# Kernel optimization log

Measured on AMD Instinct MI355X. Metric: run time of the kernel, lower is better.

Reference implementation:

```python
import jax, jax.numpy as jnp
import numpy as np

LN_EPS = 1e-5


def setup_inputs() -> dict:
    key = jax.random.key(0)
    k_h, k_s, k_d, k_w = jax.random.split(key, 4)
    N, E, F_IN, F_OUT = 100000, 1600000, 128, 128
    h = jax.random.normal(k_h, (N, F_IN), dtype=jnp.float32)
    src = jax.random.randint(k_s, (E,), 0, N, dtype=jnp.int32)
    dst = jax.random.randint(k_d, (E,), 0, N, dtype=jnp.int32)
    # Linear(2*in_feats, out_feats): weight [out, 2*in], bias [out]
    W = jax.random.normal(k_w, (F_OUT, 2 * F_IN), dtype=jnp.float32) * (1.0 / np.sqrt(2 * F_IN))
    b = jnp.zeros((F_OUT,), dtype=jnp.float32)
    gamma = jnp.ones((F_OUT,), dtype=jnp.float32)
    beta = jnp.zeros((F_OUT,), dtype=jnp.float32)
    return {"h": h, "src": src, "dst": dst, "W": W, "b": b, "gamma": gamma, "beta": beta}


def reference(h, src, dst, W, b, gamma, beta):
    N = h.shape[0]
    # mean aggregation: update_all(copy_src('h','m'), mean('m','h'))
    msg_sum = jax.ops.segment_sum(h[src], dst, num_segments=N)          # [N, F]
    deg = jax.ops.segment_sum(jnp.ones_like(dst, dtype=h.dtype), dst, num_segments=N)  # [N]
    ah = msg_sum / jnp.maximum(deg, 1.0)[:, None]                        # zero-degree -> 0 (DGL mean gives 0)
    # concat + linear
    hc = jnp.concatenate([h, ah], axis=1)                                # [N, 2F]
    z = hc @ W.T + b                                                     # [N, out]
    # LayerNorm (elementwise affine)
    mu = jnp.mean(z, axis=-1, keepdims=True)
    var = jnp.mean((z - mu) ** 2, axis=-1, keepdims=True)
    z = (z - mu) * jax.lax.rsqrt(var + LN_EPS) * gamma + beta
    # activation = relu
    return jax.nn.relu(z)
```

## Files before the change

### kernel.cpp

```cpp
#include <hip/hip_runtime.h>
#include <stdint.h>

#define FDIM 128
#define NBITS 6
#define BNODES 64
#define CAP 1536
#define PBATCH 8192

typedef __attribute__((ext_vector_type(8))) short bf16x8;
typedef __attribute__((ext_vector_type(4))) float f32x4;
typedef __attribute__((ext_vector_type(8))) unsigned short u16x8;

__device__ __forceinline__ unsigned short f32_to_bf16(float f) {
  union { float f; uint32_t u; } v; v.f = f;
  uint32_t u = v.u;
  u += 0x7FFFu + ((u >> 16) & 1u);
  return (unsigned short)(u >> 16);
}
__device__ __forceinline__ float u32lo_bf16(uint32_t u) {
  union { uint32_t u; float f; } v; v.u = u << 16; return v.f;
}
__device__ __forceinline__ float u32hi_bf16(uint32_t u) {
  union { uint32_t u; float f; } v; v.u = u & 0xFFFF0000u; return v.f;
}

__device__ __forceinline__ void gload_lds16(const void* g, void* l) {
  __builtin_amdgcn_global_load_lds(
      (const __attribute__((address_space(1))) void*)g,
      (__attribute__((address_space(3))) void*)l, 16, 0, 0);
}

__global__ void cvt_bf16_8(const float* __restrict__ in, unsigned short* __restrict__ o, int n8) {
  int i = blockIdx.x * blockDim.x + threadIdx.x;
  if (i >= n8) return;
  float4 a = ((const float4*)in)[i * 2], b = ((const float4*)in)[i * 2 + 1];
  u16x8 r;
  r[0] = f32_to_bf16(a.x); r[1] = f32_to_bf16(a.y); r[2] = f32_to_bf16(a.z); r[3] = f32_to_bf16(a.w);
  r[4] = f32_to_bf16(b.x); r[5] = f32_to_bf16(b.y); r[6] = f32_to_bf16(b.z); r[7] = f32_to_bf16(b.w);
  ((u16x8*)o)[i] = r;
}

__global__ __launch_bounds__(256) void partition_edges(
    const int* __restrict__ src, const int* __restrict__ dst,
    int* __restrict__ gcur, unsigned int* __restrict__ pairs, int E, int nbk) {
  __shared__ int hist[1600];
  for (int k = threadIdx.x; k < nbk; k += 256) hist[k] = 0;
  __syncthreads();
  int base = blockIdx.x * PBATCH;
  const int4* d4p = (const int4*)(dst + base);
  const int4* s4p = (const int4*)(src + base);
#pragma unroll
  for (int j = 0; j < PBATCH / 1024; ++j) {
    int vi = j * 256 + threadIdx.x;
    int i0 = base + vi * 4;
    if (i0 < E) {
      int4 d = d4p[vi];
      atomicAdd(&hist[d.x >> NBITS], 1);
      if (i0 + 1 < E) atomicAdd(&hist[d.y >> NBITS], 1);
      if (i0 + 2 < E) atomicAdd(&hist[d.z >> NBITS], 1);
      if (i0 + 3 < E) atomicAdd(&hist[d.w >> NBITS], 1);
    }
  }
  __syncthreads();
  for (int k = threadIdx.x; k < nbk; k += 256) {
    int c = hist[k];
    hist[k] = (c > 0) ? atomicAdd(&gcur[k], c) : 0;
  }
  __syncthreads();
#pragma unroll
  for (int j = 0; j < PBATCH / 1024; ++j) {
    int vi = j * 256 + threadIdx.x;
    int i0 = base + vi * 4;
    if (i0 < E) {
      int4 d = d4p[vi];
      int4 s = s4p[vi];
#pragma unroll
      for (int q = 0; q < 4; ++q) {
        if (i0 + q >= E) break;
        int dd = (q == 0) ? d.x : (q == 1) ? d.y : (q == 2) ? d.z : d.w;
        int ss = (q == 0) ? s.x : (q == 1) ? s.y : (q == 2) ? s.z : s.w;
        int b = dd >> NBITS;
        int pos = atomicAdd(&hist[b], 1);
        if (pos < CAP)
          pairs[(size_t)b * CAP + pos] = ((unsigned)ss << NBITS) | (unsigned)(dd & (BNODES - 1));
      }
    }
  }
}

__global__ __launch_bounds__(256) void fine_sort(
    const int* __restrict__ gcur, unsigned int* __restrict__ pairs,
    int* __restrict__ noff, int* __restrict__ ndeg, int N) {
  __shared__ int larr[CAP];
  __shared__ int sorted_[CAP];
  __shared__ int cnt[BNODES];
  __shared__ int off[BNODES];
  __shared__ int cur[BNODES];
  int b = blockIdx.x;
  int n0 = b << NBITS;
  int tid = threadIdx.x;
  int ec = gcur[b]; if (ec > CAP) ec = CAP;
  if (tid < BNODES) cnt[tid] = 0;
  unsigned int* pb = pairs + (size_t)b * CAP;
  for (int e = tid; e < ec; e += 256) larr[e] = (int)pb[e];
  __syncthreads();
  for (int e = tid; e < ec; e += 256) atomicAdd(&cnt[larr[e] & (BNODES - 1)], 1);
  __syncthreads();
  if (tid < BNODES) off[tid] = cnt[tid];
  __syncthreads();
  for (int s = 1; s < BNODES; s <<= 1) {
    int v = 0;
    if (tid < BNODES && tid >= s) v = off[tid - s];
    __syncthreads();
    if (tid < BNODES) off[tid] += v;
    __syncthreads();
  }
  if (tid < BNODES) { int e0 = off[tid] - cnt[tid]; off[tid] = e0; cur[tid] = e0; }
  __syncthreads();
  for (int e = tid; e < ec; e += 256) {
    int p = larr[e];
    int pos = atomicAdd(&cur[p & (BNODES - 1)], 1);
    sorted_[pos] = p >> NBITS;
  }
  __syncthreads();
  for (int e = tid; e < ec; e += 256) pb[e] = (unsigned int)sorted_[e];
  if (tid < BNODES) {
    int node = n0 + tid;
    if (node < N) { noff[node] = b * CAP + off[tid]; ndeg[node] = cnt[tid]; }
  }
}

__global__ __launch_bounds__(256) void gather_mean(
    const unsigned short* __restrict__ h2, const int* __restrict__ noff,
    const int* __restrict__ ndeg, const unsigned int* __restrict__ ssrc,
    unsigned short* __restrict__ ah2, int N) {
  int node = blockIdx.x * 16 + (threadIdx.x >> 4);
  int lane = threadIdx.x & 15;
  if (node >= N) return;
  int o = noff[node], d = ndeg[node];
  const uint4* h4 = (const uint4*)h2;
  float l0[4] = {0,0,0,0}, h0[4] = {0,0,0,0}, l1[4] = {0,0,0,0}, h1[4] = {0,0,0,0};
  float l2[4] = {0,0,0,0}, h2a[4] = {0,0,0,0}, l3[4] = {0,0,0,0}, h3[4] = {0,0,0,0};
  int e = 0;
  for (; e + 8 <= d; e += 8) {
    int s0 = ssrc[o + e],     s1 = ssrc[o + e + 1], s2 = ssrc[o + e + 2], s3 = ssrc[o + e + 3];
    int s4 = ssrc[o + e + 4], s5 = ssrc[o + e + 5], s6 = ssrc[o + e + 6], s7 = ssrc[o + e + 7];
    uint4 v0 = h4[(size_t)s0 * 16 + lane], v1 = h4[(size_t)s1 * 16 + lane];
    uint4 v2 = h4[(size_t)s2 * 16 + lane], v3 = h4[(size_t)s3 * 16 + lane];
    uint4 v4 = h4[(size_t)s4 * 16 + lane], v5 = h4[(size_t)s5 * 16 + lane];
    uint4 v6 = h4[(size_t)s6 * 16 + lane], v7 = h4[(size_t)s7 * 16 + lane];
    uint32_t u;
#define ACC(vv, LL, HH)                                              \
    u = vv.x; LL[0] += u32lo_bf16(u); HH[0] += u32hi_bf16(u);        \
    u = vv.y; LL[1] += u32lo_bf16(u); HH[1] += u32hi_bf16(u);        \
    u = vv.z; LL[2] += u32lo_bf16(u); HH[2] += u32hi_bf16(u);        \
    u = vv.w; LL[3] += u32lo_bf16(u); HH[3] += u32hi_bf16(u);
    ACC(v0, l0, h0) ACC(v1, l1, h1) ACC(v2, l2, h2a) ACC(v3, l3, h3)
    ACC(v4, l0, h0) ACC(v5, l1, h1) ACC(v6, l2, h2a) ACC(v7, l3, h3)
  }
  for (; e + 4 <= d; e += 4) {
    int s0 = ssrc[o + e], s1 = ssrc[o + e + 1], s2 = ssrc[o + e + 2], s3 = ssrc[o + e + 3];
    uint4 v0 = h4[(size_t)s0 * 16 + lane], v1 = h4[(size_t)s1 * 16 + lane];
    uint4 v2 = h4[(size_t)s2 * 16 + lane], v3 = h4[(size_t)s3 * 16 + lane];
    uint32_t u;
    ACC(v0, l0, h0) ACC(v1, l1, h1) ACC(v2, l2, h2a) ACC(v3, l3, h3)
  }
  for (; e < d; ++e) {
    int s0 = ssrc[o + e];
    uint4 v0 = h4[(size_t)s0 * 16 + lane];
    uint32_t u;
    ACC(v0, l0, h0)
#undef ACC
  }
  float inv = 1.0f / (float)(d > 0 ? d : 1);
  u16x8 r;
#pragma unroll
  for (int q = 0; q < 4; ++q) {
    r[2 * q]     = f32_to_bf16(((l0[q] + l1[q]) + (l2[q] + l3[q])) * inv);
    r[2 * q + 1] = f32_to_bf16(((h0[q] + h1[q]) + (h2a[q] + h3[q])) * inv);
  }
  *(u16x8*)(ah2 + (size_t)node * 128 + lane * 8) = r;
}

__global__ __launch_bounds__(256) void gemm_mfma_ln_relu(
    const unsigned short* __restrict__ h2, const unsigned short* __restrict__ ah2,
    const unsigned short* __restrict__ W2, const float* __restrict__ bias,
    const float* __restrict__ gamma, const float* __restrict__ beta,
    float* __restrict__ out, int N) {
  __shared__ unsigned short As[128 * 64];
  __shared__ unsigned short Ws[128 * 64];
  int tid = threadIdx.x;
  int w = tid >> 6, l = tid & 63;
  int lr = l & 15, lg = l >> 4;
  int n0 = blockIdx.x * 128;

  f32x4 acc[2][8];
#pragma unroll
  for (int rt = 0; rt < 2; ++rt)
#pragma unroll
    for (int ct = 0; ct < 8; ++ct) acc[rt][ct] = (f32x4){0.f, 0.f, 0.f, 0.f};

  for (int kt = 0; kt < 4; ++kt) {
    const unsigned short* abase = (kt < 2) ? h2 : ah2;
#pragma unroll
    for (int rd = 0; rd < 4; ++rd) {
      int off = rd * 4096 + tid * 16;
      int r = off >> 7;
      int s = (off >> 4) & 7;
      int ls = s ^ (r & 7);
      int gn = n0 + r; if (gn > N - 1) gn = N - 1;
      gload_lds16((const char*)abase + (size_t)gn * 256 + (size_t)(kt & 1) * 128 + ls * 16,
                  (char*)As + off);
      gload_lds16((const char*)W2 + (size_t)r * 512 + (size_t)kt * 128 + ls * 16,
                  (char*)Ws + off);
    }
    __syncthreads();

    bf16x8 aF[2][2], bF[8][2];
#pragma unroll
    for (int rt = 0; rt < 2; ++rt)
#pragma unroll
      for (int kc = 0; kc < 2; ++kc) {
        int r = w * 32 + rt * 16 + lr;
        int slot = kc * 4 + lg;
        aF[rt][kc] = *(const bf16x8*)((const char*)As + r * 128 + ((slot ^ (r & 7)) * 16));
      }
#pragma unroll
    for (int ct = 0; ct < 8; ++ct)
#pragma unroll
      for (int kc = 0; kc < 2; ++kc) {
        int r = ct * 16 + lr;
        int slot = kc * 4 + lg;
        bF[ct][kc] = *(const bf16x8*)((const char*)Ws + r * 128 + ((slot ^ (r & 7)) * 16));
      }
#pragma unroll
    for (int rt = 0; rt < 2; ++rt)
#pragma unroll
      for (int ct = 0; ct < 8; ++ct)
#pragma unroll
        for (int kc = 0; kc < 2; ++kc)
          acc[rt][ct] = __builtin_amdgcn_mfma_f32_16x16x32_bf16(
              aF[rt][kc], bF[ct][kc], acc[rt][ct], 0, 0, 0);
    __syncthreads();
  }

  float bj[8], gj[8], tj[8];
#pragma unroll
  for (int ct = 0; ct < 8; ++ct) {
    int c = ct * 16 + lr;
    bj[ct] = bias[c]; gj[ct] = gamma[c]; tj[ct] = beta[c];
  }
#pragma unroll
  for (int rt = 0; rt < 2; ++rt)
#pragma unroll
    for (int q = 0; q < 4; ++q) {
      int n = n0 + w * 32 + rt * 16 + lg * 4 + q;
      float v[8], s = 0.f, s2 = 0.f;
#pragma unroll
      for (int ct = 0; ct < 8; ++ct) {
        v[ct] = acc[rt][ct][q] + bj[ct];
        s += v[ct]; s2 += v[ct] * v[ct];
      }
#pragma unroll
      for (int off = 1; off < 16; off <<= 1) {
        s  += __shfl_xor(s, off);
        s2 += __shfl_xor(s2, off);
      }
      float mean = s * (1.f / 128.f);
      float var = s2 * (1.f / 128.f) - mean * mean;
      float rstd = rsqrtf(var + 1e-5f);
      if (n < N) {
#pragma unroll
        for (int ct = 0; ct < 8; ++ct) {
          float o = (v[ct] - mean) * rstd * gj[ct] + tj[ct];
          out[(size_t)n * FDIM + ct * 16 + lr] = fmaxf(o, 0.f);
        }
      }
    }
}

extern "C" void kernel_launch(void* const* d_in, const int* in_sizes, int n_in,
                              void* d_out, int out_size, void* d_ws, size_t ws_size,
                              hipStream_t stream) {
  const float* h     = (const float*)d_in[0];
  const int*   src   = (const int*)d_in[1];
  const int*   dst   = (const int*)d_in[2];
  const float* W     = (const float*)d_in[3];
  const float* bias  = (const float*)d_in[4];
  const float* gamma = (const float*)d_in[5];
  const float* beta  = (const float*)d_in[6];
  float* out = (float*)d_out;
  int N = in_sizes[0] / FDIM;
  int E = in_sizes[1];
  int nbk = (N + BNODES - 1) >> NBITS;

  int* gcur = (int*)d_ws;
  int* noff = (int*)((char*)d_ws + 8192);
  int* ndeg = noff + ((N + 63) / 64) * 64;
  unsigned int* pairs = (unsigned int*)(ndeg + ((N + 63) / 64) * 64);
  unsigned short* h2  = (unsigned short*)((char*)pairs + (size_t)nbk * CAP * 4);
  unsigned short* ah2 = h2 + (size_t)N * 128;
  unsigned short* W2  = ah2 + (size_t)N * 128;

  hipMemsetAsync(gcur, 0, (size_t)nbk * 4, stream);
  cvt_bf16_8<<<(N * FDIM / 8 + 255) / 256, 256, 0, stream>>>(h, h2, N * FDIM / 8);
  cvt_bf16_8<<<(FDIM * 2 * FDIM / 8 + 255) / 256, 256, 0, stream>>>(W, W2, FDIM * 2 * FDIM / 8);
  partition_edges<<<(E + PBATCH - 1) / PBATCH, 256, 0, stream>>>(src, dst, gcur, pairs, E, nbk);
  fine_sort<<<nbk, 256, 0, stream>>>(gcur, pairs, noff, ndeg, N);
  gather_mean<<<(N + 15) / 16, 256, 0, stream>>>(h2, noff, ndeg, pairs, ah2, N);
  gemm_mfma_ln_relu<<<(N + 127) / 128, 256, 0, stream>>>(h2, ah2, W2, bias, gamma, beta, out, N);
}
```

Baseline: 234.4 us.

## Replace atomic bucket partition with two-level LDS radix sort and padded gather

Result: slower. 258.5 us (+10.3%).

```diff
diff --git a/kernel.cpp b/kernel.cpp
--- a/kernel.cpp
+++ b/kernel.cpp
@@ -2,10 +2,11 @@
 #include <stdint.h>
 
 #define FDIM 128
-#define NBITS 6
-#define BNODES 64
-#define CAP 1536
+#define NB1BITS 9
+#define B1NODES 512
 #define PBATCH 8192
+#define LCAP 12288
+#define PCAP 16384
 
 typedef __attribute__((ext_vector_type(8))) short bf16x8;
 typedef __attribute__((ext_vector_type(4))) float f32x4;
@@ -40,93 +41,114 @@
   ((u16x8*)o)[i] = r;
 }
 
-__global__ __launch_bounds__(256) void partition_edges(
+__global__ __launch_bounds__(256) void l1_partition(
     const int* __restrict__ src, const int* __restrict__ dst,
-    int* __restrict__ gcur, unsigned int* __restrict__ pairs, int E, int nbk) {
-  __shared__ int hist[1600];
-  for (int k = threadIdx.x; k < nbk; k += 256) hist[k] = 0;
-  __syncthreads();
-  int base = blockIdx.x * PBATCH;
-  const int4* d4p = (const int4*)(dst + base);
-  const int4* s4p = (const int4*)(src + base);
-#pragma unroll
-  for (int j = 0; j < PBATCH / 1024; ++j) {
-    int vi = j * 256 + threadIdx.x;
-    int i0 = base + vi * 4;
-    if (i0 < E) {
-      int4 d = d4p[vi];
-      atomicAdd(&hist[d.x >> NBITS], 1);
-      if (i0 + 1 < E) atomicAdd(&hist[d.y >> NBITS], 1);
-      if (i0 + 2 < E) atomicAdd(&hist[d.z >> NBITS], 1);
-      if (i0 + 3 < E) atomicAdd(&hist[d.w >> NBITS], 1);
+    unsigned int* __restrict__ l1buf, int* __restrict__ starts, int E, int nbk1) {
+  __shared__ int hist[256];
+  __shared__ int sc[256];
+  __shared__ int cur[256];
+  __shared__ unsigned int sorted[PBATCH];
+  int tid = threadIdx.x;
+  int b0 = blockIdx.x * PBATCH;
+  int n = E - b0; if (n > PBATCH) n = PBATCH;
+  hist[tid] = 0;
+  __syncthreads();
+  for (int e = tid; e < n; e += 256) atomicAdd(&hist[dst[b0 + e] >> NB1BITS], 1);
+  __syncthreads();
+  sc[tid] = hist[tid];
+  __syncthreads();
+  for (int s = 1; s < 256; s <<= 1) {
+    int x = (tid >= s) ? sc[tid - s] : 0;
+    __syncthreads();
+    sc[tid] += x;
+    __syncthreads();
+  }
+  int excl = sc[tid] - hist[tid];
+  cur[tid] = excl;
+  __syncthreads();
+  for (int e = tid; e < n; e += 256) {
+    int d = dst[b0 + e], s = src[b0 + e];
+    int b = d >> NB1BITS;
+    int pos = atomicAdd(&cur[b], 1);
+    sorted[pos] = ((unsigned)s << NB1BITS) | (unsigned)(d & (B1NODES - 1));
+  }
+  __syncthreads();
+  unsigned int* chunk = l1buf + (size_t)blockIdx.x * PBATCH;
+  for (int e = tid; e < n; e += 256) chunk[e] = sorted[e];
+  starts[blockIdx.x * 256 + tid] = excl;
+}
+
+__global__ __launch_bounds__(256) void l2_sort(
+    const unsigned int* __restrict__ l1buf, const int* __restrict__ starts,
+    unsigned int* __restrict__ ssrc, int* __restrict__ noff, int* __restrict__ ndeg,
+    int N, int nl1b) {
+  __shared__ int sbeg[256], slen[256], scl[256];
+  __shared__ unsigned int edges[LCAP];
+  __shared__ int cnt[512], ps[512], pexcl[512], cur2[512];
+  __shared__ int ecs;
+  int b = blockIdx.x;
+  int tid = threadIdx.x;
+  int s0 = 0, len = 0;
+  if (tid < nl1b) {
+    s0 = starts[tid * 256 + b];
+    len = starts[tid * 256 + b + 1] - s0;
+  }
+  sbeg[tid] = s0; slen[tid] = len; scl[tid] = len;
+  __syncthreads();
+  for (int s = 1; s < 256; s <<= 1) {
+    int x = (tid >= s) ? scl[tid - s] : 0;
+    __syncthreads();
+    scl[tid] += x;
+    __syncthreads();
+  }
+  if (tid == 255) { int t = scl[255]; ecs = (t > LCAP) ? LCAP : t; }
+  __syncthreads();
+  int ec = ecs;
+  int wv = tid >> 6, ln = tid & 63;
+  for (int i = wv; i < nl1b; i += 4) {
+    int l = slen[i];
+    int dsto = scl[i] - l;
+    const unsigned int* seg = l1buf + (size_t)i * PBATCH + sbeg[i];
+    for (int j = ln; j < l; j += 64) {
+      int p = dsto + j;
+      if (p < LCAP) edges[p] = seg[j];
     }
   }
-  __syncthreads();
-  for (int k = threadIdx.x; k < nbk; k += 256) {
-    int c = hist[k];
-    hist[k] = (c > 0) ? atomicAdd(&gcur[k], c) : 0;
-  }
-  __syncthreads();
-#pragma unroll
-  for (int j = 0; j < PBATCH / 1024; ++j) {
-    int vi = j * 256 + threadIdx.x;
-    int i0 = base + vi * 4;
-    if (i0 < E) {
-      int4 d = d4p[vi];
-      int4 s = s4p[vi];
-#pragma unroll
-      for (int q = 0; q < 4; ++q) {
-        if (i0 + q >= E) break;
-        int dd = (q == 0) ? d.x : (q == 1) ? d.y : (q == 2) ? d.z : d.w;
-        int ss = (q == 0) ? s.x : (q == 1) ? s.y : (q == 2) ? s.z : s.w;
-        int b = dd >> NBITS;
-        int pos = atomicAdd(&hist[b], 1);
-        if (pos < CAP)
-          pairs[(size_t)b * CAP + pos] = ((unsigned)ss << NBITS) | (unsigned)(dd & (BNODES - 1));
-      }
-    }
-  }
-}
-
-__global__ __launch_bounds__(256) void fine_sort(
-    const int* __restrict__ gcur, unsigned int* __restrict__ pairs,
-    int* __restrict__ noff, int* __restrict__ ndeg, int N) {
-  __shared__ int larr[CAP];
-  __shared__ int sorted_[CAP];
-  __shared__ int cnt[BNODES];
-  __shared__ int off[BNODES];
-  __shared__ int cur[BNODES];
-  int b = blockIdx.x;
-  int n0 = b << NBITS;
-  int tid = threadIdx.x;
-  int ec = gcur[b]; if (ec > CAP) ec = CAP;
-  if (tid < BNODES) cnt[tid] = 0;
-  unsigned int* pb = pairs + (size_t)b * CAP;
-  for (int e = tid; e < ec; e += 256) larr[e] = (int)pb[e];
-  __syncthreads();
-  for (int e = tid; e < ec; e += 256) atomicAdd(&cnt[larr[e] & (BNODES - 1)], 1);
-  __syncthreads();
-  if (tid < BNODES) off[tid] = cnt[tid];
-  __syncthreads();
-  for (int s = 1; s < BNODES; s <<= 1) {
-    int v = 0;
-    if (tid < BNODES && tid >= s) v = off[tid - s];
-    __syncthreads();
-    if (tid < BNODES) off[tid] += v;
-    __syncthreads();
-  }
-  if (tid < BNODES) { int e0 = off[tid] - cnt[tid]; off[tid] = e0; cur[tid] = e0; }
-  __syncthreads();
+  cnt[tid] = 0; cnt[tid + 256] = 0;
+  __syncthreads();
+  for (int e = tid; e < ec; e += 256) atomicAdd(&cnt[edges[e] & (B1NODES - 1)], 1);
+  __syncthreads();
+  ps[tid] = (cnt[tid] + 7) & ~7;
+  ps[tid + 256] = (cnt[tid + 256] + 7) & ~7;
+  __syncthreads();
+  for (int s = 1; s < 512; s <<= 1) {
+    int i0 = tid, i1 = tid + 256;
+    int v0 = (i0 >= s) ? ps[i0 - s] : 0;
+    int v1 = (i1 >= s) ? ps[i1 - s] : 0;
+    __syncthreads();
+    ps[i0] += v0; ps[i1] += v1;
+    __syncthreads();
+  }
+  pexcl[tid] = ps[tid] - ((cnt[tid] + 7) & ~7);
+  pexcl[tid + 256] = ps[tid + 256] - ((cnt[tid + 256] + 7) & ~7);
+  cur2[tid] = pexcl[tid]; cur2[tid + 256] = pexcl[tid + 256];
+  __syncthreads();
+  unsigned int* win = ssrc + (size_t)b * PCAP;
   for (int e = tid; e < ec; e += 256) {
-    int p = larr[e];
-    int pos = atomicAdd(&cur[p & (BNODES - 1)], 1);
-    sorted_[pos] = p >> NBITS;
-  }
-  __syncthreads();
-  for (int e = tid; e < ec; e += 256) pb[e] = (unsigned int)sorted_[e];
-  if (tid < BNODES) {
-    int node = n0 + tid;
-    if (node < N) { noff[node] = b * CAP + off[tid]; ndeg[node] = cnt[tid]; }
+    unsigned int p = edges[e];
+    int nl = p & (B1NODES - 1);
+    int pos = atomicAdd(&cur2[nl], 1);
+    win[pos] = p >> NB1BITS;
+  }
+  __syncthreads();
+#pragma unroll
+  for (int hq = 0; hq < 2; ++hq) {
+    int k = tid + hq * 256;
+    int c = cnt[k], st = pexcl[k];
+    int pd = (c + 7) & ~7;
+    for (int j = c; j < pd; ++j) win[st + j] = (unsigned)N;
+    int node = b * B1NODES + k;
+    if (node < N) { noff[node] = b * PCAP + st; ndeg[node] = c; }
   }
 }
 
@@ -138,17 +160,17 @@
   int lane = threadIdx.x & 15;
   if (node >= N) return;
   int o = noff[node], d = ndeg[node];
+  int pd = (d + 7) & ~7;
   const uint4* h4 = (const uint4*)h2;
+  const uint4* ip = (const uint4*)(ssrc + o);
   float l0[4] = {0,0,0,0}, h0[4] = {0,0,0,0}, l1[4] = {0,0,0,0}, h1[4] = {0,0,0,0};
   float l2[4] = {0,0,0,0}, h2a[4] = {0,0,0,0}, l3[4] = {0,0,0,0}, h3[4] = {0,0,0,0};
-  int e = 0;
-  for (; e + 8 <= d; e += 8) {
-    int s0 = ssrc[o + e],     s1 = ssrc[o + e + 1], s2 = ssrc[o + e + 2], s3 = ssrc[o + e + 3];
-    int s4 = ssrc[o + e + 4], s5 = ssrc[o + e + 5], s6 = ssrc[o + e + 6], s7 = ssrc[o + e + 7];
-    uint4 v0 = h4[(size_t)s0 * 16 + lane], v1 = h4[(size_t)s1 * 16 + lane];
-    uint4 v2 = h4[(size_t)s2 * 16 + lane], v3 = h4[(size_t)s3 * 16 + lane];
-    uint4 v4 = h4[(size_t)s4 * 16 + lane], v5 = h4[(size_t)s5 * 16 + lane];
-    uint4 v6 = h4[(size_t)s6 * 16 + lane], v7 = h4[(size_t)s7 * 16 + lane];
+  for (int e = 0; e < pd; e += 8) {
+    uint4 ia = ip[e >> 2], ib = ip[(e >> 2) + 1];
+    uint4 v0 = h4[(size_t)ia.x * 16 + lane], v1 = h4[(size_t)ia.y * 16 + lane];
+    uint4 v2 = h4[(size_t)ia.z * 16 + lane], v3 = h4[(size_t)ia.w * 16 + lane];
+    uint4 v4 = h4[(size_t)ib.x * 16 + lane], v5 = h4[(size_t)ib.y * 16 + lane];
+    uint4 v6 = h4[(size_t)ib.z * 16 + lane], v7 = h4[(size_t)ib.w * 16 + lane];
     uint32_t u;
 #define ACC(vv, LL, HH)                                              \
     u = vv.x; LL[0] += u32lo_bf16(u); HH[0] += u32hi_bf16(u);        \
@@ -157,19 +179,6 @@
     u = vv.w; LL[3] += u32lo_bf16(u); HH[3] += u32hi_bf16(u);
     ACC(v0, l0, h0) ACC(v1, l1, h1) ACC(v2, l2, h2a) ACC(v3, l3, h3)
     ACC(v4, l0, h0) ACC(v5, l1, h1) ACC(v6, l2, h2a) ACC(v7, l3, h3)
-  }
-  for (; e + 4 <= d; e += 4) {
-    int s0 = ssrc[o + e], s1 = ssrc[o + e + 1], s2 = ssrc[o + e + 2], s3 = ssrc[o + e + 3];
-    uint4 v0 = h4[(size_t)s0 * 16 + lane], v1 = h4[(size_t)s1 * 16 + lane];
-    uint4 v2 = h4[(size_t)s2 * 16 + lane], v3 = h4[(size_t)s3 * 16 + lane];
-    uint32_t u;
-    ACC(v0, l0, h0) ACC(v1, l1, h1) ACC(v2, l2, h2a) ACC(v3, l3, h3)
-  }
-  for (; e < d; ++e) {
-    int s0 = ssrc[o + e];
-    uint4 v0 = h4[(size_t)s0 * 16 + lane];
-    uint32_t u;
-    ACC(v0, l0, h0)
 #undef ACC
   }
   float inv = 1.0f / (float)(d > 0 ? d : 1);
@@ -292,21 +301,29 @@
   float* out = (float*)d_out;
   int N = in_sizes[0] / FDIM;
   int E = in_sizes[1];
-  int nbk = (N + BNODES - 1) >> NBITS;
-
-  int* gcur = (int*)d_ws;
-  int* noff = (int*)((char*)d_ws + 8192);
-  int* ndeg = noff + ((N + 63) / 64) * 64;
-  unsigned int* pairs = (unsigned int*)(ndeg + ((N + 63) / 64) * 64);
-  unsigned short* h2  = (unsigned short*)((char*)pairs + (size_t)nbk * CAP * 4);
-  unsigned short* ah2 = h2 + (size_t)N * 128;
-  unsigned short* W2  = ah2 + (size_t)N * 128;
-
-  hipMemsetAsync(gcur, 0, (size_t)nbk * 4, stream);
+  int nl1b = (E + PBATCH - 1) / PBATCH;
+  int nbk1 = (N + B1NODES - 1) >> NB1BITS;
+
+  char* p = (char*)d_ws;
+  int* starts = (int*)p;                       p += ((size_t)nl1b * 256 + 64) * 4;
+  p = (char*)(((uintptr_t)p + 255) & ~(uintptr_t)255);
+  unsigned int* l1buf = (unsigned int*)p;      p += (size_t)nl1b * PBATCH * 4;
+  unsigned int* ssrc = (unsigned int*)p;       p += (size_t)nbk1 * PCAP * 4;
+  int* noff = (int*)p;                         p += ((size_t)N + 64) * 4;
+  p = (char*)(((uintptr_t)p + 255) & ~(uintptr_t)255);
+  int* ndeg = (int*)p;                         p += ((size_t)N + 64) * 4;
+  p = (char*)(((uintptr_t)p + 255) & ~(uintptr_t)255);
+  unsigned short* h2 = (unsigned short*)p;     p += (size_t)(N + 1) * FDIM * 2;
+  p = (char*)(((uintptr_t)p + 255) & ~(uintptr_t)255);
+  unsigned short* ah2 = (unsigned short*)p;    p += (size_t)N * FDIM * 2;
+  p = (char*)(((uintptr_t)p + 255) & ~(uintptr_t)255);
+  unsigned short* W2 = (unsigned short*)p;
+
+  hipMemsetAsync(h2 + (size_t)N * FDIM, 0, FDIM * 2, stream);
   cvt_bf16_8<<<(N * FDIM / 8 + 255) / 256, 256, 0, stream>>>(h, h2, N * FDIM / 8);
   cvt_bf16_8<<<(FDIM * 2 * FDIM / 8 + 255) / 256, 256, 0, stream>>>(W, W2, FDIM * 2 * FDIM / 8);
-  partition_edges<<<(E + PBATCH - 1) / PBATCH, 256, 0, stream>>>(src, dst, gcur, pairs, E, nbk);
-  fine_sort<<<nbk, 256, 0, stream>>>(gcur, pairs, noff, ndeg, N);
-  gather_mean<<<(N + 15) / 16, 256, 0, stream>>>(h2, noff, ndeg, pairs, ah2, N);
+  l1_partition<<<nl1b, 256, 0, stream>>>(src, dst, l1buf, starts, E, nbk1);
+  l2_sort<<<nbk1, 256, 0, stream>>>(l1buf, starts, ssrc, noff, ndeg, N, nl1b);
+  gather_mean<<<(N + 15) / 16, 256, 0, stream>>>(h2, noff, ndeg, ssrc, ah2, N);
   gemm_mfma_ln_relu<<<(N + 127) / 128, 256, 0, stream>>>(h2, ah2, W2, bias, gamma, beta, out, N);
 }
```
